# Performance work log

Measured on AMD Instinct MI355X. Metric: run time of the kernel, lower is better.

## Reference

```python
import jax, jax.numpy as jnp
import numpy as np

LN_EPS = 1e-5


def setup_inputs() -> dict:
    key = jax.random.key(0)
    ks = jax.random.split(key, 4)
    B, N, C, K = 512, 100, 256, 3
    query = jax.random.normal(ks[0], (B, N, C), dtype=jnp.float32)
    value = jax.random.normal(ks[1], (B, N, C), dtype=jnp.float32)
    # nn.Linear(C, N+K): weight stored as [out,in] in torch; here use [in,out]
    W_wl = jax.random.normal(ks[2], (C, N + K), dtype=jnp.float32) / np.sqrt(C)
    b_wl = jax.random.normal(ks[3], (N + K,), dtype=jnp.float32) * 0.01
    ln_gamma = jnp.ones((C,), dtype=jnp.float32)
    ln_beta = jnp.zeros((C,), dtype=jnp.float32)
    return {"query": query, "value": value, "W_wl": W_wl, "b_wl": b_wl,
            "ln_gamma": ln_gamma, "ln_beta": ln_beta}


def reference(query, value, W_wl, b_wl, ln_gamma, ln_beta):
    B, N, C = query.shape
    K = W_wl.shape[1] - N
    # dynamic conv weights from query: [B, N, K] depthwise + [B, N, N] pointwise
    dy = jnp.einsum('bnc,ck->bnk', query, W_wl) + b_wl
    dw = dy[:, :, :K]          # depthwise kernels, one per (b, proposal)
    pw = dy[:, :, K:]          # pointwise mixing matrix [B, N, N]
    # depthwise conv1d along C with 'same' padding (cross-correlation like torch)
    pad_l = (K - 1) // 2
    pad_r = K - 1 - pad_l
    vp = jnp.pad(value, ((0, 0), (0, 0), (pad_l, pad_r)))
    depth = jnp.zeros_like(value)
    for k in range(K):  # K is tiny (3): static unrolled loop
        depth = depth + dw[:, :, k:k + 1] * vp[:, :, k:k + C]
    depth = jax.nn.relu(depth)
    # pointwise conv (kernel size 1) == per-sample NxN mix over proposals
    out = jnp.einsum('bnm,bmc->bnc', pw, depth)
    # LayerNorm over C
    mu = jnp.mean(out, axis=-1, keepdims=True)
    var = jnp.var(out, axis=-1, keepdims=True)
    out = (out - mu) * jax.lax.rsqrt(var + LN_EPS) * ln_gamma + ln_beta
    return out
```

## Files before the change

kernel.cpp:

```cpp
#include <hip/hip_runtime.h>

#define NN 100
#define CC 256
#define NKK 103
#define LSA 72
#define LDPW 136
#define OTS 260

typedef __bf16 bf16;
typedef __bf16 bf16x4 __attribute__((ext_vector_type(4)));
typedef __bf16 bf16x8 __attribute__((ext_vector_type(8)));
typedef float f32x4 __attribute__((ext_vector_type(4)));

__global__ void wl_transpose(const float* __restrict__ W, bf16* __restrict__ Wt)
{
    int idx = blockIdx.x * 256 + threadIdx.x;
    if (idx < NKK * CC) {
        int ka = idx >> 8;
        int k  = idx & 255;
        Wt[ka * CC + k] = (bf16)W[k * NKK + ka];
    }
}

__global__ __launch_bounds__(512, 4)
void dysepconv_fused(const float* __restrict__ query,
                     const float* __restrict__ value,
                     const bf16*  __restrict__ Wt,
                     const float* __restrict__ bwl,
                     const float* __restrict__ gamma,
                     const float* __restrict__ beta,
                     float* __restrict__ out)
{
    __shared__ __align__(16) char SMEM[50000];
    bf16*  PW   = (bf16*)SMEM;
    bf16*  Abuf = (bf16*)(SMEM + 27200);
    float (*DW)[3]      = (float(*)[3])(SMEM + 41600);
    float (*RP)[NN][2]  = (float(*)[NN][2])(SMEM + 42800);
    float (*RS)[2]      = (float(*)[2])(SMEM + 49200);
    float* OT = (float*)SMEM;

    const int t    = threadIdx.x;
    const int w    = t >> 6;
    const int lane = t & 63;
    const int ln16 = lane & 15;
    const int g    = lane >> 4;
    const int hi8  = g * 8;
    const int b    = blockIdx.x;
    const int cb   = w * 16 + ln16;

    const float* qb = query + (size_t)b * NN * CC;
    const float* vb = value + (size_t)b * NN * CC;

    f32x4 acc1[7];
    #pragma unroll
    for (int I = 0; I < 7; ++I) acc1[I] = (f32x4){0.f, 0.f, 0.f, 0.f};

    const int rB = (w * 16 + ln16 < NKK) ? (w * 16 + ln16) : (NKK - 1);
    bf16x8 wfrag[4][2];
    #pragma unroll
    for (int kc = 0; kc < 4; ++kc)
        #pragma unroll
        for (int s = 0; s < 2; ++s)
            wfrag[kc][s] = *(const bf16x8*)(Wt + rB * CC + kc * 64 + s * 32 + hi8);

    f32x4 qv[4];
    #pragma unroll
    for (int p = 0; p < 4; ++p) {
        int idx = p * 512 + t;
        if (idx < 1600) {
            int r = idx >> 4, j = (idx & 15) << 2;
            qv[p] = *(const f32x4*)(qb + r * CC + j);
        }
    }

    #pragma unroll
    for (int kc = 0; kc < 4; ++kc) {
        if (kc) __syncthreads();
        #pragma unroll
        for (int p = 0; p < 4; ++p) {
            int idx = p * 512 + t;
            if (idx < 1600) {
                int r = idx >> 4, j = (idx & 15) << 2;
                bf16x4 s;
                #pragma unroll
                for (int i = 0; i < 4; ++i) s[i] = (bf16)qv[p][i];
                *(bf16x4*)&Abuf[r * LSA + j] = s;
            }
        }
        f32x4 qn[4];
        if (kc < 3) {
            #pragma unroll
            for (int p = 0; p < 4; ++p) {
                int idx = p * 512 + t;
                if (idx < 1600) {
                    int r = idx >> 4, j = (idx & 15) << 2;
                    qn[p] = *(const f32x4*)(qb + r * CC + (kc + 1) * 64 + j);
                }
            }
        }
        __syncthreads();

        if (w < 7) {
            #pragma unroll
            for (int s = 0; s < 2; ++s) {
                bf16x8 bv = wfrag[kc][s];
                #pragma unroll
                for (int I = 0; I < 7; ++I) {
                    int row = I * 16 + ln16;
                    row = (row < NN) ? row : (NN - 1);
                    bf16x8 av = *(const bf16x8*)&Abuf[row * LSA + s * 32 + hi8];
                    acc1[I] = __builtin_amdgcn_mfma_f32_16x16x32_bf16(av, bv, acc1[I], 0, 0, 0);
                }
            }
        }
        if (kc < 3) {
            #pragma unroll
            for (int p = 0; p < 4; ++p) qv[p] = qn[p];
        }
    }

    for (int i = t; i < NN * 28; i += 512) {
        int r = i / 28, m = 100 + (i - (i / 28) * 28);
        PW[r * LDPW + m] = (bf16)0.f;
    }
    float xv[8], yv[8];
    #pragma unroll
    for (int j = 0; j < 8; ++j) {
        int m = hi8 + j;
        const float* vr = vb + m * CC;
        xv[j] = vr[cb];
        yv[j] = vr[cb + 128];
    }
    if (w < 7) {
        const int kap = w * 16 + ln16;
        const float bw = (kap < NKK) ? bwl[kap] : 0.f;
        #pragma unroll
        for (int I = 0; I < 7; ++I) {
            #pragma unroll
            for (int r = 0; r < 4; ++r) {
                int n = I * 16 + g * 4 + r;
                if (n < NN && kap < NKK) {
                    float v = acc1[I][r] + bw;
                    if (kap < 3) DW[n][kap] = v;
                    else         PW[n * LDPW + (kap - 3)] = (bf16)v;
                }
            }
        }
    }
    __syncthreads();

    f32x4 acc2[2][7];
    #pragma unroll
    for (int st = 0; st < 2; ++st)
        #pragma unroll
        for (int I = 0; I < 7; ++I) acc2[st][I] = (f32x4){0.f, 0.f, 0.f, 0.f};

    #pragma unroll
    for (int ks = 0; ks < 4; ++ks) {
        float xn[8], yn[8];
        if (ks < 3) {
            #pragma unroll
            for (int j = 0; j < 8; ++j) {
                int m = (ks + 1) * 32 + hi8 + j;
                bool mv = (m < NN);
                const float* vr = vb + m * CC;
                xn[j] = mv ? vr[cb]       : 0.f;
                yn[j] = mv ? vr[cb + 128] : 0.f;
            }
        }
        bf16x8 dv0, dv1;
        #pragma unroll
        for (int j = 0; j < 8; ++j) {
            int  m  = ks * 32 + hi8 + j;
            bool mv = (m < NN);
            int  mc = mv ? m : (NN - 1);
            float w0 = DW[mc][0], w1 = DW[mc][1], w2 = DW[mc][2];
            float x0 = xv[j], y0 = yv[j];
            float xm = __shfl(x0, (lane - 1) & 63), xp = __shfl(x0, (lane + 1) & 63);
            float ym = __shfl(y0, (lane - 1) & 63), yp = __shfl(y0, (lane + 1) & 63);
            if (ln16 == 0) {
                xm = (mv && cb > 0) ? vb[m * CC + cb - 1] : 0.f;
                ym = mv ? vb[m * CC + cb + 127] : 0.f;
            }
            if (ln16 == 15) {
                xp = mv ? vb[m * CC + cb + 1] : 0.f;
                yp = (mv && cb + 129 < CC) ? vb[m * CC + cb + 129] : 0.f;
            }
            float d0 = w0 * xm + w1 * x0 + w2 * xp;
            float d1 = w0 * ym + w1 * y0 + w2 * yp;
            dv0[j] = (bf16)(mv ? fmaxf(d0, 0.f) : 0.f);
            dv1[j] = (bf16)(mv ? fmaxf(d1, 0.f) : 0.f);
        }
        #pragma unroll
        for (int I = 0; I < 7; ++I) {
            int row = I * 16 + ln16;
            row = (row < NN) ? row : (NN - 1);
            bf16x8 af = *(const bf16x8*)&PW[row * LDPW + ks * 32 + hi8];
            acc2[0][I] = __builtin_amdgcn_mfma_f32_16x16x32_bf16(af, dv0, acc2[0][I], 0, 0, 0);
            acc2[1][I] = __builtin_amdgcn_mfma_f32_16x16x32_bf16(af, dv1, acc2[1][I], 0, 0, 0);
        }
        if (ks < 3) {
            #pragma unroll
            for (int j = 0; j < 8; ++j) { xv[j] = xn[j]; yv[j] = yn[j]; }
        }
    }

    const float gm0 = gamma[cb], gm1 = gamma[cb + 128];
    const float bt0 = beta[cb],  bt1 = beta[cb + 128];

    #pragma unroll
    for (int I = 0; I < 7; ++I) {
        #pragma unroll
        for (int r = 0; r < 4; ++r) {
            float a = acc2[0][I][r], e = acc2[1][I][r];
            float s1 = a + e, s2 = a * a + e * e;
            #pragma unroll
            for (int mk = 1; mk < 16; mk <<= 1) {
                s1 += __shfl_xor(s1, mk);
                s2 += __shfl_xor(s2, mk);
            }
            int n = I * 16 + g * 4 + r;
            if (ln16 == 0 && n < NN) {
                RP[w][n][0] = s1;
                RP[w][n][1] = s2;
            }
        }
    }
    __syncthreads();
    if (t < NN) {
        float S1 = 0.f, S2 = 0.f;
        #pragma unroll
        for (int wi = 0; wi < 8; ++wi) { S1 += RP[wi][t][0]; S2 += RP[wi][t][1]; }
        float mu  = S1 * (1.f / 256.f);
        float var = S2 * (1.f / 256.f) - mu * mu;
        RS[t][0] = mu;
        RS[t][1] = rsqrtf(fmaxf(var, 0.f) + 1e-5f);
    }
    __syncthreads();

    float* ob = out + (size_t)b * NN * CC;
    #pragma unroll
    for (int h = 0; h < 3; ++h) {
        const int n0   = h * 40;
        const int rows = (h == 2) ? 20 : 40;
        #pragma unroll
        for (int I = 0; I < 7; ++I) {
            #pragma unroll
            for (int r = 0; r < 4; ++r) {
                int n = I * 16 + g * 4 + r;
                if (n >= n0 && n < n0 + rows) {
                    float mu = RS[n][0], rs = RS[n][1];
                    int rt = n - n0;
                    OT[rt * OTS + cb]       = (acc2[0][I][r] - mu) * rs * gm0 + bt0;
                    OT[rt * OTS + cb + 128] = (acc2[1][I][r] - mu) * rs * gm1 + bt1;
                }
            }
        }
        __syncthreads();
        #pragma unroll
        for (int p = 0; p < 5; ++p) {
            int idx = p * 512 + t;
            if (idx < rows * 64) {
                int row = idx >> 6, c4 = (idx & 63) << 2;
                *(f32x4*)(ob + (size_t)(n0 + row) * CC + c4) = *(const f32x4*)&OT[row * OTS + c4];
            }
        }
        if (h < 2) __syncthreads();
    }
}

extern "C" void kernel_launch(void* const* d_in, const int* in_sizes, int n_in,
                              void* d_out, int out_size, void* d_ws, size_t ws_size,
                              hipStream_t stream) {
    const float* query = (const float*)d_in[0];
    const float* value = (const float*)d_in[1];
    const float* W     = (const float*)d_in[2];
    const float* bwl   = (const float*)d_in[3];
    const float* gamma = (const float*)d_in[4];
    const float* beta  = (const float*)d_in[5];
    bf16* Wt = (bf16*)d_ws;

    wl_transpose<<<dim3((NKK * CC + 255) / 256), dim3(256), 0, stream>>>(W, Wt);
    dysepconv_fused<<<dim3(512), dim3(512), 0, stream>>>(query, value, Wt, bwl, gamma, beta, (float*)d_out);
}
```

Measured before the change: 197.5 us.

## Load weight fragments per chunk and drop value prefetch registers

The weight fragments for the first GEMM are no longer preloaded into 8 vector registers up front. Each K-chunk now loads its two fragments just in time. The software-prefetch double buffer for value rows in the pointwise stage is also removed, so values load at the start of each iteration. The aim is to lower VGPR pressure, which helps the kernel meet its launch bounds of 512 threads and 4 blocks, at the cost of exposing global-load latency that was previously hidden.

Measured after the change: 189.6 us. 4.0% less time.

```diff
diff --git a/kernel.cpp b/kernel.cpp
--- a/kernel.cpp
+++ b/kernel.cpp
@@ -56,12 +56,6 @@
     for (int I = 0; I < 7; ++I) acc1[I] = (f32x4){0.f, 0.f, 0.f, 0.f};
 
     const int rB = (w * 16 + ln16 < NKK) ? (w * 16 + ln16) : (NKK - 1);
-    bf16x8 wfrag[4][2];
-    #pragma unroll
-    for (int kc = 0; kc < 4; ++kc)
-        #pragma unroll
-        for (int s = 0; s < 2; ++s)
-            wfrag[kc][s] = *(const bf16x8*)(Wt + rB * CC + kc * 64 + s * 32 + hi8);
 
     f32x4 qv[4];
     #pragma unroll
@@ -87,6 +81,8 @@
                 *(bf16x4*)&Abuf[r * LSA + j] = s;
             }
         }
+        bf16x8 wf0 = *(const bf16x8*)(Wt + rB * CC + kc * 64 + hi8);
+        bf16x8 wf1 = *(const bf16x8*)(Wt + rB * CC + kc * 64 + 32 + hi8);
         f32x4 qn[4];
         if (kc < 3) {
             #pragma unroll
@@ -102,15 +98,18 @@
 
         if (w < 7) {
             #pragma unroll
-            for (int s = 0; s < 2; ++s) {
-                bf16x8 bv = wfrag[kc][s];
-                #pragma unroll
-                for (int I = 0; I < 7; ++I) {
-                    int row = I * 16 + ln16;
-                    row = (row < NN) ? row : (NN - 1);
-                    bf16x8 av = *(const bf16x8*)&Abuf[row * LSA + s * 32 + hi8];
-                    acc1[I] = __builtin_amdgcn_mfma_f32_16x16x32_bf16(av, bv, acc1[I], 0, 0, 0);
-                }
+            for (int I = 0; I < 7; ++I) {
+                int row = I * 16 + ln16;
+                row = (row < NN) ? row : (NN - 1);
+                bf16x8 av = *(const bf16x8*)&Abuf[row * LSA + hi8];
+                acc1[I] = __builtin_amdgcn_mfma_f32_16x16x32_bf16(av, wf0, acc1[I], 0, 0, 0);
+            }
+            #pragma unroll
+            for (int I = 0; I < 7; ++I) {
+                int row = I * 16 + ln16;
+                row = (row < NN) ? row : (NN - 1);
+                bf16x8 av = *(const bf16x8*)&Abuf[row * LSA + 32 + hi8];
+                acc1[I] = __builtin_amdgcn_mfma_f32_16x16x32_bf16(av, wf1, acc1[I], 0, 0, 0);
             }
         }
         if (kc < 3) {
@@ -157,15 +156,14 @@
 
     #pragma unroll
     for (int ks = 0; ks < 4; ++ks) {
-        float xn[8], yn[8];
-        if (ks < 3) {
+        if (ks) {
             #pragma unroll
             for (int j = 0; j < 8; ++j) {
-                int m = (ks + 1) * 32 + hi8 + j;
+                int m = ks * 32 + hi8 + j;
                 bool mv = (m < NN);
                 const float* vr = vb + m * CC;
-                xn[j] = mv ? vr[cb]       : 0.f;
-                yn[j] = mv ? vr[cb + 128] : 0.f;
+                xv[j] = mv ? vr[cb]       : 0.f;
+                yv[j] = mv ? vr[cb + 128] : 0.f;
             }
         }
         bf16x8 dv0, dv1;
@@ -199,10 +197,6 @@
             acc2[0][I] = __builtin_amdgcn_mfma_f32_16x16x32_bf16(af, dv0, acc2[0][I], 0, 0, 0);
             acc2[1][I] = __builtin_amdgcn_mfma_f32_16x16x32_bf16(af, dv1, acc2[1][I], 0, 0, 0);
         }
-        if (ks < 3) {
-            #pragma unroll
-            for (int j = 0; j < 8; ++j) { xv[j] = xn[j]; yv[j] = yn[j]; }
-        }
     }
 
     const float gm0 = gamma[cb], gm1 = gamma[cb + 128];
```
